# Performance work log

Measured on AMD Instinct MI355X. Metric: run time of the kernel, lower is better.

## Reference

```python
import jax, jax.numpy as jnp
import numpy as np

B, S, D = 1, 2048, 1024   # batch, seq_len, d_model
E, F, TOP_K = 8, 4096, 2  # num_experts, d_ff, top_k


def setup_inputs() -> dict:
    key = jax.random.key(0)
    k0, k1, k2, k3, k4 = jax.random.split(key, 5)
    s = 0.02
    x = jax.random.normal(k0, (B, S, D), jnp.float32)
    Wr = jax.random.normal(k1, (D, E), jnp.float32) * s          # router
    W1 = jax.random.normal(k2, (E, D, F), jnp.float32) * s       # gate proj per expert
    W3 = jax.random.normal(k3, (E, D, F), jnp.float32) * s       # up proj per expert
    W2 = jax.random.normal(k4, (E, F, D), jnp.float32) * s       # down proj per expert
    return {"x": x, "Wr": Wr, "W1": W1, "W2": W2, "W3": W3}


def reference(x, Wr, W1, W2, W3):
    b, s, d = x.shape
    e = Wr.shape[1]
    xt = x.reshape(b * s, d)                       # [T, D]
    logits = xt @ Wr                               # [T, E]
    top_v, top_i = jax.lax.top_k(logits, TOP_K)    # [T, K]
    probs = jax.nn.softmax(top_v, axis=-1)         # softmax over selected experts
    # combine[t, e] = prob of expert e for token t (0 if not selected)
    combine = jnp.sum(probs[..., None] * jax.nn.one_hot(top_i, e, dtype=xt.dtype), axis=1)  # [T, E]
    # SwiGLU FFN per expert (dense grouped-GEMM form of the gather/scatter loop)
    h = jnp.einsum('td,edf->etf', xt, W1)          # [E, T, F]
    g = jnp.einsum('td,edf->etf', xt, W3)          # [E, T, F]
    y = jnp.einsum('etf,efd->etd', jax.nn.silu(h) * g, W2)  # [E, T, D]
    out = jnp.einsum('etd,te->td', y, combine)     # weighted combine
    return out.reshape(b, s, d)
```

## Files before the change

### kernel.cpp

```cpp
#include <hip/hip_runtime.h>
#include <hip/hip_bf16.h>

#define T_TOK 2048
#define DDIM  1024
#define NEXP  8
#define FDIM  4096

typedef __attribute__((ext_vector_type(8))) short bf16x8;
typedef __attribute__((ext_vector_type(4))) float f32x4;

#define SBW(n) ((((n) >> 3) ^ (n)) & 7)

__device__ __forceinline__ unsigned short f2b(float f) {
  union { float f; unsigned u; } v; v.f = f;
  unsigned r = v.u + 0x7FFF + ((v.u >> 16) & 1);
  return (unsigned short)(r >> 16);
}
__device__ __forceinline__ float b2f(unsigned short s) {
  union { unsigned u; float f; } v; v.u = ((unsigned)s) << 16;
  return v.f;
}
__device__ __forceinline__ unsigned cvtpk(float lo, float hi) {
  unsigned r;
  asm("v_cvt_pk_bf16_f32 %0, %1, %2" : "=v"(r) : "v"(lo), "v"(hi));
  return r;
}
__device__ __forceinline__ void gl16(const unsigned short* g, unsigned short* l) {
  __builtin_amdgcn_global_load_lds(
      (const __attribute__((address_space(1))) unsigned int*)(const void*)g,
      (__attribute__((address_space(3))) unsigned int*)(void*)l, 16, 0, 0);
}
__device__ __forceinline__ bf16x8 pack8(const float4* br, int c) {
  union { bf16x8 v; unsigned u[4]; } p;
  p.u[0] = cvtpk((&br[0].x)[c], (&br[1].x)[c]);
  p.u[1] = cvtpk((&br[2].x)[c], (&br[3].x)[c]);
  p.u[2] = cvtpk((&br[4].x)[c], (&br[5].x)[c]);
  p.u[3] = cvtpk((&br[6].x)[c], (&br[7].x)[c]);
  return p.v;
}

__global__ void router_kernel(const float* __restrict__ x, const float* __restrict__ Wr,
                              int* __restrict__ cnt, int* __restrict__ tok,
                              float* __restrict__ prb) {
  int t = (blockIdx.x * blockDim.x + threadIdx.x) >> 6;
  int lane = threadIdx.x & 63;
  if (t >= T_TOK) return;
  const float* xr = x + (size_t)t * DDIM;
  float acc[NEXP];
#pragma unroll
  for (int e = 0; e < NEXP; ++e) acc[e] = 0.f;
#pragma unroll
  for (int i = 0; i < 4; ++i) {
    int d0 = lane * 16 + i * 4;
    float4 xv = *reinterpret_cast<const float4*>(xr + d0);
#pragma unroll
    for (int j = 0; j < 4; ++j) {
      float xd = (&xv.x)[j];
      float4 w0 = *reinterpret_cast<const float4*>(Wr + (size_t)(d0 + j) * NEXP);
      float4 w1 = *reinterpret_cast<const float4*>(Wr + (size_t)(d0 + j) * NEXP + 4);
      acc[0] += xd * w0.x; acc[1] += xd * w0.y; acc[2] += xd * w0.z; acc[3] += xd * w0.w;
      acc[4] += xd * w1.x; acc[5] += xd * w1.y; acc[6] += xd * w1.z; acc[7] += xd * w1.w;
    }
  }
#pragma unroll
  for (int off = 32; off >= 1; off >>= 1)
#pragma unroll
    for (int e = 0; e < NEXP; ++e) acc[e] += __shfl_down(acc[e], off);
  if (lane == 0) {
    float v0 = -1e30f, v1 = -1e30f; int i0 = 0, i1 = 0;
#pragma unroll
    for (int e = 0; e < NEXP; ++e) {
      float v = acc[e];
      if (v > v0)      { v1 = v0; i1 = i0; v0 = v; i0 = e; }
      else if (v > v1) { v1 = v; i1 = e; }
    }
    float e1 = __expf(v1 - v0);
    float p0 = 1.f / (1.f + e1);
    float p1 = e1 * p0;
    int s0 = atomicAdd(&cnt[i0], 1);
    tok[i0 * T_TOK + s0] = t; prb[i0 * T_TOK + s0] = p0;
    int s1 = atomicAdd(&cnt[i1], 1);
    tok[i1 * T_TOK + s1] = t; prb[i1 * T_TOK + s1] = p1;
  }
}

__global__ void cvt_x_kernel(const float* __restrict__ in, unsigned short* __restrict__ o) {
  size_t i = ((size_t)blockIdx.x * 256 + threadIdx.x) * 8;
  float4 a = *reinterpret_cast<const float4*>(in + i);
  float4 b = *reinterpret_cast<const float4*>(in + i + 4);
  bf16x8 p;
  p[0] = (short)f2b(a.x); p[1] = (short)f2b(a.y); p[2] = (short)f2b(a.z); p[3] = (short)f2b(a.w);
  p[4] = (short)f2b(b.x); p[5] = (short)f2b(b.y); p[6] = (short)f2b(b.z); p[7] = (short)f2b(b.w);
  *reinterpret_cast<bf16x8*>(o + i) = p;
}

__global__ __launch_bounds__(256, 3)
void gemm1ab_kernel(const unsigned short* __restrict__ xb,
                    const float* __restrict__ W1, const float* __restrict__ W3,
                    const int* __restrict__ cnt, const int* __restrict__ tok,
                    unsigned short* __restrict__ act) {
  const int e = blockIdx.z;
  const int cn = cnt[e];
  const int r0 = blockIdx.y * 128;
  if (r0 >= cn) return;
  const int n0 = blockIdx.x * 64;
  int off = 0;
#pragma unroll
  for (int i = 0; i < NEXP; ++i) off += (i < e) ? cnt[i] : 0;

  __shared__ __align__(16) unsigned short sA[128 * 64];
  __shared__ __align__(16) unsigned short sB1[64 * 64];
  __shared__ __align__(16) unsigned short sB3[64 * 64];

  const int tid = threadIdx.x;
  const int lane = tid & 63;
  const int wid = tid >> 6;
  const int wm = wid >> 1, wn = wid & 1;

  const unsigned short* asrc[4];
#pragma unroll
  for (int i = 0; i < 4; ++i) {
    int row = (4 * wid + i) * 8 + (lane >> 3);
    int slot = r0 + row; if (slot >= cn) slot = cn - 1;
    int tk = tok[e * T_TOK + slot];
    int sl = (lane & 7) ^ (row & 7);
    asrc[i] = xb + (size_t)tk * DDIM + sl * 8;
  }

  const int lt = tid & 127;
  const int ko = lt >> 4;
  const int nc = (lt & 15) * 4;
  const float* bp = ((tid < 128) ? W1 : W3) + ((size_t)e * DDIM + 8 * ko) * FDIM + n0 + nc;
  unsigned short* wb = (tid < 128) ? sB1 : sB3;
  int woff[4];
#pragma unroll
  for (int c = 0; c < 4; ++c) woff[c] = (nc + c) * 64 + ((ko ^ SBW(nc + c)) * 8);

  float4 br[8];
#define LOADB1(K0)                                                              \
  _Pragma("unroll") for (int r = 0; r < 8; ++r)                                 \
      br[r] = *reinterpret_cast<const float4*>(bp + (size_t)((K0) + r) * FDIM);
#define WRITEB1()                                                               \
  _Pragma("unroll") for (int c = 0; c < 4; ++c)                                 \
      *reinterpret_cast<bf16x8*>(wb + woff[c]) = pack8(br, c);
#define STAGEA1(K0)                                                             \
  _Pragma("unroll") for (int i = 0; i < 4; ++i)                                 \
      gl16(asrc[i] + (K0), &sA[(4 * wid + i) * 512]);

  f32x4 ah[4][2], ag[4][2];
#pragma unroll
  for (int m = 0; m < 4; ++m)
#pragma unroll
    for (int n = 0; n < 2; ++n) { ah[m][n] = (f32x4){0,0,0,0}; ag[m][n] = (f32x4){0,0,0,0}; }

  LOADB1(0);

  for (int k0 = 0; k0 < DDIM; k0 += 64) {
    WRITEB1();
    STAGEA1(k0);
    __syncthreads();
    if (k0 + 64 < DDIM) LOADB1(k0 + 64);
#pragma unroll
    for (int kk = 0; kk < 2; ++kk) {
      int kc8 = kk * 4 + (lane >> 4);
      bf16x8 a[4], b1[2], b3[2];
#pragma unroll
      for (int m = 0; m < 4; ++m) {
        int row = wm * 64 + m * 16 + (lane & 15);
        a[m] = *reinterpret_cast<const bf16x8*>(&sA[row * 64 + ((kc8 ^ (row & 7)) * 8)]);
      }
#pragma unroll
      for (int n = 0; n < 2; ++n) {
        int rowb = wn * 32 + n * 16 + (lane & 15);
        int offb = rowb * 64 + ((kc8 ^ SBW(rowb)) * 8);
        b1[n] = *reinterpret_cast<const bf16x8*>(&sB1[offb]);
        b3[n] = *reinterpret_cast<const bf16x8*>(&sB3[offb]);
      }
#pragma unroll
      for (int m = 0; m < 4; ++m)
#pragma unroll
        for (int n = 0; n < 2; ++n) {
          ah[m][n] = __builtin_amdgcn_mfma_f32_16x16x32_bf16(a[m], b1[n], ah[m][n], 0, 0, 0);
          ag[m][n] = __builtin_amdgcn_mfma_f32_16x16x32_bf16(a[m], b3[n], ag[m][n], 0, 0, 0);
        }
    }
    __syncthreads();
  }
#pragma unroll
  for (int m = 0; m < 4; ++m)
#pragma unroll
    for (int j = 0; j < 4; ++j) {
      int rloc = wm * 64 + m * 16 + (lane >> 4) * 4 + j;
      int s = r0 + rloc;
      if (s < cn) {
        unsigned short* orow = act + (size_t)(off + s) * FDIM + n0 + wn * 32 + (lane & 15);
#pragma unroll
        for (int n = 0; n < 2; ++n) {
          float hv = ah[m][n][j];
          float gv = ag[m][n][j];
          float sg = hv / (1.f + __expf(-hv));
          orow[n * 16] = f2b(sg * gv);
        }
      }
    }
}

__global__ __launch_bounds__(256, 3)
void gemm2d_kernel(const unsigned short* __restrict__ act, const float* __restrict__ W2,
                   const int* __restrict__ cnt, const int* __restrict__ tok,
                   const float* __restrict__ prb, float* __restrict__ out) {
  const int e = blockIdx.z >> 2;
  const int sp = blockIdx.z & 3;
  const int cn = cnt[e];
  const int r0 = blockIdx.y * 128;
  if (r0 >= cn) return;
  const int n0 = blockIdx.x * 128;
  const int kbase = sp * (FDIM / 4);
  int off = 0;
#pragma unroll
  for (int i = 0; i < NEXP; ++i) off += (i < e) ? cnt[i] : 0;

  __shared__ __align__(16) unsigned short sA[128 * 64];
  __shared__ __align__(16) unsigned short sB[128 * 64];

  const int tid = threadIdx.x;
  const int lane = tid & 63;
  const int wid = tid >> 6;
  const int wm = wid >> 1, wn = wid & 1;

  const unsigned short* asrc[4];
#pragma unroll
  for (int i = 0; i < 4; ++i) {
    int row = (4 * wid + i) * 8 + (lane >> 3);
    int sl = (lane & 7) ^ (row & 7);
    asrc[i] = act + (size_t)(off + r0 + row) * FDIM + kbase + sl * 8;
  }

  const int ko = tid >> 5;
  const int nc = (tid & 31) * 4;
  const float* bp = W2 + ((size_t)e * FDIM + kbase + 8 * ko) * DDIM + n0 + nc;
  int woff[4];
#pragma unroll
  for (int c = 0; c < 4; ++c) woff[c] = (nc + c) * 64 + ((ko ^ SBW(nc + c)) * 8);

  float4 br[8];
#define LOADB2(K0)                                                              \
  _Pragma("unroll") for (int r = 0; r < 8; ++r)                                 \
      br[r] = *reinterpret_cast<const float4*>(bp + (size_t)((K0) + r) * DDIM);
#define WRITEB2()                                                               \
  _Pragma("unroll") for (int c = 0; c < 4; ++c)                                 \
      *reinterpret_cast<bf16x8*>(&sB[woff[c]]) = pack8(br, c);
#define STAGEA2(K0)                                                             \
  _Pragma("unroll") for (int i = 0; i < 4; ++i)                                 \
      gl16(asrc[i] + (K0), &sA[(4 * wid + i) * 512]);

  f32x4 acc[4][4];
#pragma unroll
  for (int m = 0; m < 4; ++m)
#pragma unroll
    for (int n = 0; n < 4; ++n) acc[m][n] = (f32x4){0,0,0,0};

  LOADB2(0);

  for (int k0 = 0; k0 < FDIM / 4; k0 += 64) {
    WRITEB2();
    STAGEA2(k0);
    __syncthreads();
    if (k0 + 64 < FDIM / 4) LOADB2(k0 + 64);
#pragma unroll
    for (int kk = 0; kk < 2; ++kk) {
      int kc8 = kk * 4 + (lane >> 4);
      bf16x8 a[4], b[4];
#pragma unroll
      for (int m = 0; m < 4; ++m) {
        int row = wm * 64 + m * 16 + (lane & 15);
        a[m] = *reinterpret_cast<const bf16x8*>(&sA[row * 64 + ((kc8 ^ (row & 7)) * 8)]);
      }
#pragma unroll
      for (int n = 0; n < 4; ++n) {
        int col = wn * 64 + n * 16 + (lane & 15);
        b[n] = *reinterpret_cast<const bf16x8*>(&sB[col * 64 + ((kc8 ^ SBW(col)) * 8)]);
      }
#pragma unroll
      for (int m = 0; m < 4; ++m)
#pragma unroll
        for (int n = 0; n < 4; ++n)
          acc[m][n] = __builtin_amdgcn_mfma_f32_16x16x32_bf16(a[m], b[n], acc[m][n], 0, 0, 0);
    }
    __syncthreads();
  }
#pragma unroll
  for (int m = 0; m < 4; ++m)
#pragma unroll
    for (int j = 0; j < 4; ++j) {
      int rloc = wm * 64 + m * 16 + (lane >> 4) * 4 + j;
      int s = r0 + rloc;
      if (s < cn) {
        int tkn = tok[e * T_TOK + s];
        float p = prb[e * T_TOK + s];
        float* orow = out + (size_t)tkn * DDIM + n0 + wn * 64 + (lane & 15);
#pragma unroll
        for (int n = 0; n < 4; ++n) atomicAdd(&orow[n * 16], p * acc[m][n][j]);
      }
    }
}

extern "C" void kernel_launch(void* const* d_in, const int* in_sizes, int n_in,
                              void* d_out, int out_size, void* d_ws, size_t ws_size,
                              hipStream_t stream) {
  const float* x  = (const float*)d_in[0];
  const float* Wr = (const float*)d_in[1];
  const float* W1 = (const float*)d_in[2];
  const float* W2 = (const float*)d_in[3];
  const float* W3 = (const float*)d_in[4];
  float* out = (float*)d_out;

  char* ws = (char*)d_ws;
  int*   cnt = (int*)ws;
  int*   tok = (int*)(ws + 1024);
  float* prb = (float*)(ws + 1024 + 65536);
  unsigned short* xb  = (unsigned short*)(ws + 256 * 1024);
  unsigned short* act = xb + (size_t)T_TOK * DDIM;

  hipMemsetAsync(cnt, 0, NEXP * sizeof(int), stream);
  hipMemsetAsync(d_out, 0, (size_t)out_size * sizeof(float), stream);

  router_kernel<<<T_TOK / 4, 256, 0, stream>>>(x, Wr, cnt, tok, prb);
  cvt_x_kernel<<<(T_TOK * DDIM) / (256 * 8), 256, 0, stream>>>(x, xb);
  gemm1ab_kernel<<<dim3(FDIM / 64, 16, NEXP), 256, 0, stream>>>(xb, W1, W3, cnt, tok, act);
  gemm2d_kernel<<<dim3(DDIM / 128, 16, NEXP * 4), 256, 0, stream>>>(act, W2, cnt, tok, prb, out);
}
```

Baseline: 297.1 us.

## Make gate/up GEMM weight-stationary: hold full-K weight slice in LDS

Replaces the tiled gate/up GEMM with a weight-stationary kernel. Each 512-thread block converts a 32-column, full-K slice of W1 and W3 for one expert into LDS once, then loops over that expert's tokens in chunks of 512. The A operand (the gathered bf16 activations) is read straight from global memory without LDS staging or per-k syncs. This is meant to cut redundant fp32 weight reads and conversions across row-tiles, at the cost of one block per CU (128KB LDS), gather loads from global memory that are not coalesced, and serialised token chunks for heavily loaded experts.

```diff
diff --git a/kernel.cpp b/kernel.cpp
--- a/kernel.cpp
+++ b/kernel.cpp
@@ -5,6 +5,7 @@
 #define DDIM  1024
 #define NEXP  8
 #define FDIM  4096
+#define ROWS  (4096 + 256)
 
 typedef __attribute__((ext_vector_type(8))) short bf16x8;
 typedef __attribute__((ext_vector_type(4))) float f32x4;
@@ -94,87 +95,86 @@
   *reinterpret_cast<bf16x8*>(o + i) = p;
 }
 
-__global__ __launch_bounds__(256, 3)
-void gemm1ab_kernel(const unsigned short* __restrict__ xb,
-                    const float* __restrict__ W1, const float* __restrict__ W3,
-                    const int* __restrict__ cnt, const int* __restrict__ tok,
-                    unsigned short* __restrict__ act) {
+__global__ __launch_bounds__(512, 1)
+void ffn1s_kernel(const unsigned short* __restrict__ xb,
+                  const float* __restrict__ W1, const float* __restrict__ W3,
+                  const int* __restrict__ cnt, const int* __restrict__ tok,
+                  unsigned short* __restrict__ act) {
   const int e = blockIdx.z;
+  const int p = blockIdx.x;
   const int cn = cnt[e];
-  const int r0 = blockIdx.y * 128;
-  if (r0 >= cn) return;
-  const int n0 = blockIdx.x * 64;
+  if (cn <= 0) return;
   int off = 0;
 #pragma unroll
   for (int i = 0; i < NEXP; ++i) off += (i < e) ? cnt[i] : 0;
 
-  __shared__ __align__(16) unsigned short sA[128 * 64];
-  __shared__ __align__(16) unsigned short sB1[64 * 64];
-  __shared__ __align__(16) unsigned short sB3[64 * 64];
+  __shared__ __align__(16) unsigned short sW[2][32 * 1024];
 
   const int tid = threadIdx.x;
   const int lane = tid & 63;
-  const int wid = tid >> 6;
-  const int wm = wid >> 1, wn = wid & 1;
-
-  const unsigned short* asrc[4];
-#pragma unroll
-  for (int i = 0; i < 4; ++i) {
-    int row = (4 * wid + i) * 8 + (lane >> 3);
-    int slot = r0 + row; if (slot >= cn) slot = cn - 1;
-    int tk = tok[e * T_TOK + slot];
-    int sl = (lane & 7) ^ (row & 7);
-    asrc[i] = xb + (size_t)tk * DDIM + sl * 8;
-  }
-
-  const int lt = tid & 127;
-  const int ko = lt >> 4;
-  const int nc = (lt & 15) * 4;
-  const float* bp = ((tid < 128) ? W1 : W3) + ((size_t)e * DDIM + 8 * ko) * FDIM + n0 + nc;
-  unsigned short* wb = (tid < 128) ? sB1 : sB3;
-  int woff[4];
-#pragma unroll
-  for (int c = 0; c < 4; ++c) woff[c] = (nc + c) * 64 + ((ko ^ SBW(nc + c)) * 8);
-
-  float4 br[8];
-#define LOADB1(K0)                                                              \
-  _Pragma("unroll") for (int r = 0; r < 8; ++r)                                 \
-      br[r] = *reinterpret_cast<const float4*>(bp + (size_t)((K0) + r) * FDIM);
-#define WRITEB1()                                                               \
-  _Pragma("unroll") for (int c = 0; c < 4; ++c)                                 \
-      *reinterpret_cast<bf16x8*>(wb + woff[c]) = pack8(br, c);
-#define STAGEA1(K0)                                                             \
-  _Pragma("unroll") for (int i = 0; i < 4; ++i)                                 \
-      gl16(asrc[i] + (K0), &sA[(4 * wid + i) * 512]);
-
-  f32x4 ah[4][2], ag[4][2];
-#pragma unroll
-  for (int m = 0; m < 4; ++m)
-#pragma unroll
-    for (int n = 0; n < 2; ++n) { ah[m][n] = (f32x4){0,0,0,0}; ag[m][n] = (f32x4){0,0,0,0}; }
-
-  LOADB1(0);
-
-  for (int k0 = 0; k0 < DDIM; k0 += 64) {
-    WRITEB1();
-    STAGEA1(k0);
-    __syncthreads();
-    if (k0 + 64 < DDIM) LOADB1(k0 + 64);
-#pragma unroll
-    for (int kk = 0; kk < 2; ++kk) {
-      int kc8 = kk * 4 + (lane >> 4);
+  const int w = tid >> 6;
+
+  {
+    const int m01 = tid >> 8;
+    const int t = tid & 255;
+    const int np = (t & 15) * 2;
+    const int kg = (t >> 4) * 8;
+    const float* src = (m01 ? W3 : W1) + (size_t)e * DDIM * FDIM + p * 32 + np;
+    unsigned short* dst = &sW[m01][0];
+#pragma unroll
+    for (int it = 0; it < 8; ++it) {
+      int kb = it * 128 + kg;
+      float2 br2[8];
+#pragma unroll
+      for (int r = 0; r < 8; ++r)
+        br2[r] = *reinterpret_cast<const float2*>(src + (size_t)(kb + r) * FDIM);
+      int s = kb >> 3;
+#pragma unroll
+      for (int c = 0; c < 2; ++c) {
+        int n = np + c;
+        union { bf16x8 v; unsigned u[4]; } pk;
+        pk.u[0] = cvtpk((&br2[0].x)[c], (&br2[1].x)[c]);
+        pk.u[1] = cvtpk((&br2[2].x)[c], (&br2[3].x)[c]);
+        pk.u[2] = cvtpk((&br2[4].x)[c], (&br2[5].x)[c]);
+        pk.u[3] = cvtpk((&br2[6].x)[c], (&br2[7].x)[c]);
+        *reinterpret_cast<bf16x8*>(&dst[n * 1024 + ((s ^ (n & 7)) << 3)]) = pk.v;
+      }
+    }
+  }
+  __syncthreads();
+
+  const int lq = lane >> 4;
+  const int ln = lane & 15;
+
+  const int nch = (cn + 511) >> 9;
+  for (int ch = 0; ch < nch; ++ch) {
+    const unsigned short* ab[4];
+#pragma unroll
+    for (int m = 0; m < 4; ++m) {
+      int row = ch * 512 + w * 64 + m * 16 + ln;
+      int slot = row < cn ? row : cn - 1;
+      int tk = tok[e * T_TOK + slot];
+      ab[m] = xb + (size_t)tk * DDIM + lq * 8;
+    }
+
+    f32x4 ah[4][2], ag[4][2];
+#pragma unroll
+    for (int m = 0; m < 4; ++m)
+#pragma unroll
+      for (int n = 0; n < 2; ++n) { ah[m][n] = (f32x4){0,0,0,0}; ag[m][n] = (f32x4){0,0,0,0}; }
+
+#pragma unroll 8
+    for (int kk = 0; kk < 32; ++kk) {
       bf16x8 a[4], b1[2], b3[2];
 #pragma unroll
-      for (int m = 0; m < 4; ++m) {
-        int row = wm * 64 + m * 16 + (lane & 15);
-        a[m] = *reinterpret_cast<const bf16x8*>(&sA[row * 64 + ((kc8 ^ (row & 7)) * 8)]);
-      }
+      for (int m = 0; m < 4; ++m)
+        a[m] = *reinterpret_cast<const bf16x8*>(ab[m] + kk * 32);
 #pragma unroll
       for (int n = 0; n < 2; ++n) {
-        int rowb = wn * 32 + n * 16 + (lane & 15);
-        int offb = rowb * 64 + ((kc8 ^ SBW(rowb)) * 8);
-        b1[n] = *reinterpret_cast<const bf16x8*>(&sB1[offb]);
-        b3[n] = *reinterpret_cast<const bf16x8*>(&sB3[offb]);
+        int row = n * 16 + ln;
+        int sl = (((kk * 4 + lq) ^ (row & 7)) << 3);
+        b1[n] = *reinterpret_cast<const bf16x8*>(&sW[0][row * 1024 + sl]);
+        b3[n] = *reinterpret_cast<const bf16x8*>(&sW[1][row * 1024 + sl]);
       }
 #pragma unroll
       for (int m = 0; m < 4; ++m)
@@ -184,25 +184,24 @@
           ag[m][n] = __builtin_amdgcn_mfma_f32_16x16x32_bf16(a[m], b3[n], ag[m][n], 0, 0, 0);
         }
     }
-    __syncthreads();
-  }
-#pragma unroll
-  for (int m = 0; m < 4; ++m)
-#pragma unroll
-    for (int j = 0; j < 4; ++j) {
-      int rloc = wm * 64 + m * 16 + (lane >> 4) * 4 + j;
-      int s = r0 + rloc;
-      if (s < cn) {
-        unsigned short* orow = act + (size_t)(off + s) * FDIM + n0 + wn * 32 + (lane & 15);
-#pragma unroll
-        for (int n = 0; n < 2; ++n) {
-          float hv = ah[m][n][j];
-          float gv = ag[m][n][j];
-          float sg = hv / (1.f + __expf(-hv));
-          orow[n * 16] = f2b(sg * gv);
+
+#pragma unroll
+    for (int m = 0; m < 4; ++m)
+#pragma unroll
+      for (int j = 0; j < 4; ++j) {
+        int s = ch * 512 + w * 64 + m * 16 + lq * 4 + j;
+        if (s < cn) {
+          unsigned short* orow = act + (size_t)(off + s) * FDIM + p * 32 + ln;
+#pragma unroll
+          for (int n = 0; n < 2; ++n) {
+            float hv = ah[m][n][j];
+            float gv = ag[m][n][j];
+            float sg = hv / (1.f + __expf(-hv));
+            orow[n * 16] = f2b(sg * gv);
+          }
         }
       }
-    }
+  }
 }
 
 __global__ __launch_bounds__(256, 3)
@@ -327,6 +326,6 @@
 
   router_kernel<<<T_TOK / 4, 256, 0, stream>>>(x, Wr, cnt, tok, prb);
   cvt_x_kernel<<<(T_TOK * DDIM) / (256 * 8), 256, 0, stream>>>(x, xb);
-  gemm1ab_kernel<<<dim3(FDIM / 64, 16, NEXP), 256, 0, stream>>>(xb, W1, W3, cnt, tok, act);
+  ffn1s_kernel<<<dim3(FDIM / 32, 1, NEXP), 512, 0, stream>>>(xb, W1, W3, cnt, tok, act);
   gemm2d_kernel<<<dim3(DDIM / 128, 16, NEXP * 4), 256, 0, stream>>>(act, W2, cnt, tok, prb, out);
 }
```

Result: slower. 380.7 us (+28.2%).

## Pre-gather routed tokens into expert-contiguous bf16 buffer; halve down-proj K split

Applied to the files above, without the earlier changes.

Replaces the full-x bf16 conversion with a gather kernel that writes each routed token's row, converted to bf16, into a per-expert contiguous buffer. GEMM1 can then stage A with linear addressing instead of indirect token lookups. The down-projection split-K factor drops from 4 to 2, which halves the atomic accumulation into the output but also halves the number of blocks. The gather loop reads rows beyond cnt at expert boundaries and relies on a padded buffer (ROWS) for tail tiles.

```diff
diff --git a/kernel.cpp b/kernel.cpp
--- a/kernel.cpp
+++ b/kernel.cpp
@@ -5,6 +5,7 @@
 #define DDIM  1024
 #define NEXP  8
 #define FDIM  4096
+#define ROWS  (4096 + 256)
 
 typedef __attribute__((ext_vector_type(8))) short bf16x8;
 typedef __attribute__((ext_vector_type(4))) float f32x4;
@@ -84,20 +85,34 @@
   }
 }
 
-__global__ void cvt_x_kernel(const float* __restrict__ in, unsigned short* __restrict__ o) {
-  size_t i = ((size_t)blockIdx.x * 256 + threadIdx.x) * 8;
-  float4 a = *reinterpret_cast<const float4*>(in + i);
-  float4 b = *reinterpret_cast<const float4*>(in + i + 4);
-  bf16x8 p;
-  p[0] = (short)f2b(a.x); p[1] = (short)f2b(a.y); p[2] = (short)f2b(a.z); p[3] = (short)f2b(a.w);
-  p[4] = (short)f2b(b.x); p[5] = (short)f2b(b.y); p[6] = (short)f2b(b.z); p[7] = (short)f2b(b.w);
-  *reinterpret_cast<bf16x8*>(o + i) = p;
+__global__ void gather_x_kernel(const float* __restrict__ x, const int* __restrict__ cnt,
+                                const int* __restrict__ tok, unsigned short* __restrict__ xg) {
+  int gs = blockIdx.x * 4 + (threadIdx.x >> 6);
+  int lane = threadIdx.x & 63;
+  int s = gs, e = 0;
+#pragma unroll
+  for (int i = 0; i < NEXP - 1; ++i) {
+    int c = cnt[i];
+    bool go = (e == i) && (s >= c);
+    if (go) { s -= c; e = i + 1; }
+  }
+  int tk = tok[e * T_TOK + s];
+  const float* src = x + (size_t)tk * DDIM;
+  unsigned short* dst = xg + (size_t)gs * DDIM;
+#pragma unroll
+  for (int it = 0; it < 4; ++it) {
+    float4 v = *reinterpret_cast<const float4*>(src + it * 256 + lane * 4);
+    uint2 p;
+    p.x = cvtpk(v.x, v.y);
+    p.y = cvtpk(v.z, v.w);
+    *reinterpret_cast<uint2*>(dst + it * 256 + lane * 4) = p;
+  }
 }
 
 __global__ __launch_bounds__(256, 3)
-void gemm1ab_kernel(const unsigned short* __restrict__ xb,
+void gemm1ab_kernel(const unsigned short* __restrict__ xg,
                     const float* __restrict__ W1, const float* __restrict__ W3,
-                    const int* __restrict__ cnt, const int* __restrict__ tok,
+                    const int* __restrict__ cnt,
                     unsigned short* __restrict__ act) {
   const int e = blockIdx.z;
   const int cn = cnt[e];
@@ -121,10 +136,8 @@
 #pragma unroll
   for (int i = 0; i < 4; ++i) {
     int row = (4 * wid + i) * 8 + (lane >> 3);
-    int slot = r0 + row; if (slot >= cn) slot = cn - 1;
-    int tk = tok[e * T_TOK + slot];
     int sl = (lane & 7) ^ (row & 7);
-    asrc[i] = xb + (size_t)tk * DDIM + sl * 8;
+    asrc[i] = xg + (size_t)(off + r0 + row) * DDIM + sl * 8;
   }
 
   const int lt = tid & 127;
@@ -209,13 +222,13 @@
 void gemm2d_kernel(const unsigned short* __restrict__ act, const float* __restrict__ W2,
                    const int* __restrict__ cnt, const int* __restrict__ tok,
                    const float* __restrict__ prb, float* __restrict__ out) {
-  const int e = blockIdx.z >> 2;
-  const int sp = blockIdx.z & 3;
+  const int e = blockIdx.z >> 1;
+  const int sp = blockIdx.z & 1;
   const int cn = cnt[e];
   const int r0 = blockIdx.y * 128;
   if (r0 >= cn) return;
   const int n0 = blockIdx.x * 128;
-  const int kbase = sp * (FDIM / 4);
+  const int kbase = sp * (FDIM / 2);
   int off = 0;
 #pragma unroll
   for (int i = 0; i < NEXP; ++i) off += (i < e) ? cnt[i] : 0;
@@ -262,11 +275,11 @@
 
   LOADB2(0);
 
-  for (int k0 = 0; k0 < FDIM / 4; k0 += 64) {
+  for (int k0 = 0; k0 < FDIM / 2; k0 += 64) {
     WRITEB2();
     STAGEA2(k0);
     __syncthreads();
-    if (k0 + 64 < FDIM / 4) LOADB2(k0 + 64);
+    if (k0 + 64 < FDIM / 2) LOADB2(k0 + 64);
 #pragma unroll
     for (int kk = 0; kk < 2; ++kk) {
       int kc8 = kk * 4 + (lane >> 4);
@@ -319,14 +332,14 @@
   int*   cnt = (int*)ws;
   int*   tok = (int*)(ws + 1024);
   float* prb = (float*)(ws + 1024 + 65536);
-  unsigned short* xb  = (unsigned short*)(ws + 256 * 1024);
-  unsigned short* act = xb + (size_t)T_TOK * DDIM;
+  unsigned short* xg  = (unsigned short*)(ws + 256 * 1024);
+  unsigned short* act = xg + (size_t)ROWS * DDIM;
 
   hipMemsetAsync(cnt, 0, NEXP * sizeof(int), stream);
   hipMemsetAsync(d_out, 0, (size_t)out_size * sizeof(float), stream);
 
   router_kernel<<<T_TOK / 4, 256, 0, stream>>>(x, Wr, cnt, tok, prb);
-  cvt_x_kernel<<<(T_TOK * DDIM) / (256 * 8), 256, 0, stream>>>(x, xb);
-  gemm1ab_kernel<<<dim3(FDIM / 64, 16, NEXP), 256, 0, stream>>>(xb, W1, W3, cnt, tok, act);
-  gemm2d_kernel<<<dim3(DDIM / 128, 16, NEXP * 4), 256, 0, stream>>>(act, W2, cnt, tok, prb, out);
-}
+  gather_x_kernel<<<(2 * T_TOK) / 4, 256, 0, stream>>>(x, cnt, tok, xg);
+  gemm1ab_kernel<<<dim3(FDIM / 64, 16, NEXP), 256, 0, stream>>>(xg, W1, W3, cnt, act);
+  gemm2d_kernel<<<dim3(DDIM / 128, 16, NEXP * 2), 256, 0, stream>>>(act, W2, cnt, tok, prb, out);
+}
```

New measurement: 294.7 us. About the same (-0.8%).
